# Kernel optimization log

Hardware: AMD Instinct MI355X
Metric: run time of the kernel (lower is better)

Reference implementation:

```python
import jax, jax.numpy as jnp
import numpy as np

H = 2048
EPS = 1e-5

def _layernorm(x, g, b):
    mu = jnp.mean(x, axis=-1, keepdims=True)
    var = jnp.mean(jnp.square(x - mu), axis=-1, keepdims=True)
    return (x - mu) * jax.lax.rsqrt(var + EPS) * g + b

def setup_inputs() -> dict:
    key = jax.random.key(0)
    ks = jax.random.split(key, 12)
    s = 1.0 / np.sqrt(H)
    inp = {
        "x": jax.random.normal(ks[0], (2, 2048, H), dtype=jnp.float32),
        "ln1_g": jnp.ones((H,), jnp.float32),
        "ln1_b": jnp.zeros((H,), jnp.float32),
        "ln2_g": jnp.ones((H,), jnp.float32),
        "ln2_b": jnp.zeros((H,), jnp.float32),
        "qkv_w": jax.random.uniform(ks[1], (H, 3 * H), jnp.float32, -s, s),
        "qkv_b": jax.random.uniform(ks[2], (3 * H,), jnp.float32, -s, s),
        "out_w": jax.random.uniform(ks[3], (H, H), jnp.float32, -s, s),
        "out_b": jax.random.uniform(ks[4], (H,), jnp.float32, -s, s),
        "mlp_w1": jax.random.uniform(ks[5], (H, 4 * H), jnp.float32, -s, s),
        "mlp_b1": jax.random.uniform(ks[6], (4 * H,), jnp.float32, -s, s),
        "mlp_w2": jax.random.uniform(ks[7], (4 * H, H), jnp.float32, -1.0 / np.sqrt(4 * H), 1.0 / np.sqrt(4 * H)),
        "mlp_b2": jax.random.uniform(ks[8], (H,), jnp.float32, -1.0 / np.sqrt(4 * H), 1.0 / np.sqrt(4 * H)),
    }
    return inp

def reference(x, ln1_g, ln1_b, ln2_g, ln2_b, qkv_w, qkv_b, out_w, out_b, mlp_w1, mlp_b1, mlp_w2, mlp_b2):
    residual = x
    h = _layernorm(x, ln1_g, ln1_b)
    qkv = h @ qkv_w + qkv_b                      # [B,S,3H]
    q, k, v = jnp.split(qkv, 3, axis=-1)         # each [B,S,H] (single-head attention)
    scores = jnp.einsum('bsh,bth->bst', q, k) / jnp.sqrt(jnp.float32(H))
    attn = jax.nn.softmax(scores, axis=-1)
    attn_out = jnp.einsum('bst,bth->bsh', attn, v)
    attn_out = attn_out @ out_w + out_b
    x = residual + attn_out                      # dropout is identity in eval
    residual = x
    h = _layernorm(x, ln2_g, ln2_b)
    h = jax.nn.gelu(h @ mlp_w1 + mlp_b1, approximate=False)
    h = h @ mlp_w2 + mlp_b2
    return residual + h
```

## Files before the change

kernel.cpp:

```cpp
#include <hip/hip_runtime.h>
#include <hip/hip_bf16.h>
#include <math.h>

typedef __bf16 bf16_t;
typedef __bf16 bf16x8 __attribute__((ext_vector_type(8)));
typedef __bf16 bf16x4 __attribute__((ext_vector_type(4)));
typedef float  f32x4  __attribute__((ext_vector_type(4)));

enum { EPI_BF16_BIAS = 0, EPI_F32_SCALE = 1, EPI_BF16 = 2, EPI_F32_BIAS_RES = 3, EPI_BF16_BIAS_GELU = 4 };

__device__ __forceinline__ float gelu_exact(float v) {
  return 0.5f * v * (1.0f + erff(v * 0.7071067811865476f));
}

__device__ __forceinline__ void gld_lds16(const bf16_t* g, bf16_t* l) {
  __builtin_amdgcn_global_load_lds(
      (const __attribute__((address_space(1))) uint32_t*)(uintptr_t)g,
      (__attribute__((address_space(3))) uint32_t*)(uintptr_t)l, 16, 0, 0);
}

#define SB()    __builtin_amdgcn_s_barrier()
#define SCHED() __builtin_amdgcn_sched_barrier(0)
#define VMW0()  asm volatile("s_waitcnt vmcnt(0)" ::: "memory")

template<int EPI, int ZDIV>
__global__ __launch_bounds__(512, 2) void tb_gemm8(
    const bf16_t* __restrict__ A, int lda, long long strideA, long long kofA,
    const bf16_t* __restrict__ B, int ldb, long long strideB, long long kofB,
    const float* __restrict__ bias,
    const float* __restrict__ resid,
    void* __restrict__ Cp, int ldc, long long strideC,
    int K, float scale)
{
  __shared__ __align__(16) bf16_t sm[65536];

  const int tid = threadIdx.x;
  const int lane = tid & 63;
  const int wid = tid >> 6;
  const int wm = wid >> 2;
  const int wn = wid & 3;
  const int lr = lane & 15;
  const int lg = lane >> 4;
  const int z = blockIdx.z;
  const int batch = z / ZDIV;
  const int ks = z % ZDIV;
  const int m0 = blockIdx.y * 256;
  const int n0 = blockIdx.x * 256;

  const bf16_t* Ag = A + (size_t)batch * strideA + (size_t)ks * kofA + (size_t)m0 * lda;
  const bf16_t* Bg = B + (size_t)batch * strideB + (size_t)ks * kofB + (size_t)n0 * ldb;

  const int l3 = lane >> 3;
  const int sl8 = ((lane & 7) ^ l3) << 3;

  f32x4 acc[8][4];
#pragma unroll
  for (int i = 0; i < 8; ++i)
#pragma unroll
    for (int j = 0; j < 4; ++j) acc[i][j] = (f32x4){0.f, 0.f, 0.f, 0.f};

  auto stage = [&](int par, int kt) {
    bf16_t* da = sm + (par << 15);
    bf16_t* db = da + 16384;
#pragma unroll
    for (int h = 0; h < 2; ++h)
#pragma unroll
      for (int q = 0; q < 2; ++q) {
        int c = (wid << 1) + q;
        int row = (h << 7) + (c << 3) + l3;
        gld_lds16(Ag + (size_t)row * lda + kt + sl8, da + (h << 13) + (c << 9) + lane * 8);
        gld_lds16(Bg + (size_t)row * ldb + kt + sl8, db + (h << 13) + (c << 9) + lane * 8);
      }
  };

#define RD(base, rowbase, kslot) \
  (*(const bf16x8*)((base) + ((rowbase) + lr) * 64 + (((((kslot) << 2) | lg)) ^ (lr & 7)) * 8))

  const int NT = K >> 6;
  stage(0, 0);
  VMW0();
  SB();

  for (int t = 0; t < NT; ++t) {
    SCHED();
    const bf16_t* cura = sm + ((t & 1) << 15);
    const bf16_t* curb = cura + 16384;
    if (t + 1 < NT) stage((t + 1) & 1, (t + 1) << 6);

    bf16x8 bF[4][2], aF[4][2];
#pragma unroll
    for (int jj = 0; jj < 4; ++jj) {
      bF[jj][0] = RD(curb, jj * 64 + wn * 16, 0);
      bF[jj][1] = RD(curb, jj * 64 + wn * 16, 1);
    }
#pragma unroll
    for (int ii = 0; ii < 4; ++ii) {
      aF[ii][0] = RD(cura, ii * 32 + wm * 16, 0);
      aF[ii][1] = RD(cura, ii * 32 + wm * 16, 1);
    }
    __builtin_amdgcn_s_setprio(1);
#pragma unroll
    for (int ii = 0; ii < 4; ++ii)
#pragma unroll
      for (int jj = 0; jj < 4; ++jj)
#pragma unroll
        for (int kk = 0; kk < 2; ++kk)
          acc[ii][jj] = __builtin_amdgcn_mfma_f32_16x16x32_bf16(aF[ii][kk], bF[jj][kk], acc[ii][jj], 0, 0, 0);
    __builtin_amdgcn_s_setprio(0);
#pragma unroll
    for (int ii = 0; ii < 4; ++ii) {
      aF[ii][0] = RD(cura, 128 + ii * 32 + wm * 16, 0);
      aF[ii][1] = RD(cura, 128 + ii * 32 + wm * 16, 1);
    }
    __builtin_amdgcn_s_setprio(1);
#pragma unroll
    for (int ii = 0; ii < 4; ++ii)
#pragma unroll
      for (int jj = 0; jj < 4; ++jj)
#pragma unroll
        for (int kk = 0; kk < 2; ++kk)
          acc[4 + ii][jj] = __builtin_amdgcn_mfma_f32_16x16x32_bf16(aF[ii][kk], bF[jj][kk], acc[4 + ii][jj], 0, 0, 0);
    __builtin_amdgcn_s_setprio(0);

    SCHED();
    if (t + 1 < NT) {
      VMW0();
      SB();
    }
  }
#undef RD

#pragma unroll
  for (int i = 0; i < 8; ++i) {
    const int mr = ((i >> 2) << 7) + ((i & 3) << 5) + (wm << 4);
#pragma unroll
    for (int j = 0; j < 4; ++j) {
      const int nc = j * 64 + (wn << 4);
#pragma unroll
      for (int r = 0; r < 4; ++r) {
        int row = m0 + mr + lg * 4 + r;
        int col = n0 + nc + lr;
        float v = acc[i][j][r] * scale;
        if constexpr (EPI == EPI_BF16_BIAS || EPI == EPI_F32_BIAS_RES || EPI == EPI_BF16_BIAS_GELU)
          v += bias[col];
        if constexpr (EPI == EPI_BF16_BIAS_GELU)
          v = gelu_exact(v);
        if constexpr (EPI == EPI_F32_BIAS_RES)
          v += resid[(size_t)row * ldc + col];
        if constexpr (EPI == EPI_BF16_BIAS || EPI == EPI_BF16 || EPI == EPI_BF16_BIAS_GELU) {
          ((bf16_t*)Cp)[(size_t)z * strideC + (size_t)row * ldc + col] = (bf16_t)v;
        } else {
          ((float*)Cp)[(size_t)z * strideC + (size_t)row * ldc + col] = v;
        }
      }
    }
  }
}

__global__ __launch_bounds__(256) void tb_combine(
    const float* __restrict__ x2, const float* __restrict__ p0,
    const float* __restrict__ p1, const float* __restrict__ bias,
    float* __restrict__ out)
{
  size_t o = ((size_t)blockIdx.x * 256 + threadIdx.x) * 4;
  float4 a = *(const float4*)(x2 + o);
  float4 b = *(const float4*)(p0 + o);
  float4 c = *(const float4*)(p1 + o);
  float4 bb = *(const float4*)(bias + (o & 2047));
  float4 r;
  r.x = a.x + b.x + c.x + bb.x;
  r.y = a.y + b.y + c.y + bb.y;
  r.z = a.z + b.z + c.z + bb.z;
  r.w = a.w + b.w + c.w + bb.w;
  *(float4*)(out + o) = r;
}

__global__ __launch_bounds__(256) void tb_combine_pv(
    const float* __restrict__ p, bf16_t* __restrict__ ao)
{
  size_t o = ((size_t)blockIdx.x * 256 + threadIdx.x) * 4;
  size_t b = o >> 22;
  size_t w = o & 4194303;
  const float* p0 = p + (b << 1) * 4194304 + w;
  const float* p1 = p0 + 4194304;
  float4 a = *(const float4*)p0;
  float4 c = *(const float4*)p1;
  bf16x4 r;
  r[0] = (bf16_t)(a.x + c.x);
  r[1] = (bf16_t)(a.y + c.y);
  r[2] = (bf16_t)(a.z + c.z);
  r[3] = (bf16_t)(a.w + c.w);
  *(bf16x4*)(ao + o) = r;
}

__global__ __launch_bounds__(256) void tb_transpose_cast(
    const float* __restrict__ in, bf16_t* __restrict__ outT, int R, int C)
{
  __shared__ float tile[32][33];
  int c0 = blockIdx.x * 32;
  int r0 = blockIdx.y * 32;
  int t = threadIdx.x;
  int r = t >> 3;
  int c4 = (t & 7) * 4;
  float4 d = *(const float4*)(in + (size_t)(r0 + r) * C + c0 + c4);
  tile[r][c4 + 0] = d.x; tile[r][c4 + 1] = d.y; tile[r][c4 + 2] = d.z; tile[r][c4 + 3] = d.w;
  __syncthreads();
  int c = t >> 3;
  int r4 = (t & 7) * 4;
  bf16x4 o;
  o[0] = (bf16_t)tile[r4 + 0][c];
  o[1] = (bf16_t)tile[r4 + 1][c];
  o[2] = (bf16_t)tile[r4 + 2][c];
  o[3] = (bf16_t)tile[r4 + 3][c];
  *(bf16x4*)(outT + (size_t)(c0 + c) * R + r0 + r4) = o;
}

__global__ __launch_bounds__(256) void tb_transpose_bf16(
    const bf16_t* __restrict__ in, int ldin, long long sIn,
    bf16_t* __restrict__ out, int ldout, long long sOut)
{
  __shared__ bf16_t tile[32][40];
  int z = blockIdx.z;
  const bf16_t* src = in + (size_t)z * sIn;
  bf16_t* dst = out + (size_t)z * sOut;
  int c0 = blockIdx.x * 32;
  int r0 = blockIdx.y * 32;
  int t = threadIdx.x;
  int r = t >> 3;
  int c4 = (t & 7) * 4;
  bf16x4 d = *(const bf16x4*)(src + (size_t)(r0 + r) * ldin + c0 + c4);
  *(bf16x4*)&tile[r][c4] = d;
  __syncthreads();
  int c = t >> 3;
  int r4 = (t & 7) * 4;
  bf16x4 o;
  o[0] = tile[r4 + 0][c];
  o[1] = tile[r4 + 1][c];
  o[2] = tile[r4 + 2][c];
  o[3] = tile[r4 + 3][c];
  *(bf16x4*)(dst + (size_t)(c0 + c) * ldout + r0 + r4) = o;
}

__global__ __launch_bounds__(256) void tb_layernorm(
    const float* __restrict__ x, const float* __restrict__ g, const float* __restrict__ b,
    bf16_t* __restrict__ h)
{
  __shared__ float sa[4], sb[4];
  int row = blockIdx.x;
  int t = threadIdx.x;
  const float* xr = x + (size_t)row * 2048;
  float4 v0 = *(const float4*)(xr + t * 8);
  float4 v1 = *(const float4*)(xr + t * 8 + 4);
  float a[8] = {v0.x, v0.y, v0.z, v0.w, v1.x, v1.y, v1.z, v1.w};
  float s = 0.f, q = 0.f;
#pragma unroll
  for (int j = 0; j < 8; ++j) { s += a[j]; q += a[j] * a[j]; }
#pragma unroll
  for (int o = 32; o; o >>= 1) { s += __shfl_down(s, o); q += __shfl_down(q, o); }
  int w = t >> 6, l = t & 63;
  if (l == 0) { sa[w] = s; sb[w] = q; }
  __syncthreads();
  if (t == 0) {
    sa[0] = sa[0] + sa[1] + sa[2] + sa[3];
    sb[0] = sb[0] + sb[1] + sb[2] + sb[3];
  }
  __syncthreads();
  float mu = sa[0] * (1.0f / 2048.0f);
  float var = sb[0] * (1.0f / 2048.0f) - mu * mu;
  float rs = rsqrtf(var + 1e-5f);
  float4 g0 = *(const float4*)(g + t * 8);
  float4 g1 = *(const float4*)(g + t * 8 + 4);
  float4 b0 = *(const float4*)(b + t * 8);
  float4 b1 = *(const float4*)(b + t * 8 + 4);
  float gv[8] = {g0.x, g0.y, g0.z, g0.w, g1.x, g1.y, g1.z, g1.w};
  float bv[8] = {b0.x, b0.y, b0.z, b0.w, b1.x, b1.y, b1.z, b1.w};
  bf16x8 o8;
#pragma unroll
  for (int j = 0; j < 8; ++j) o8[j] = (bf16_t)((a[j] - mu) * rs * gv[j] + bv[j]);
  *(bf16x8*)(h + (size_t)row * 2048 + t * 8) = o8;
}

__global__ __launch_bounds__(256) void tb_softmax_add(
    const float* __restrict__ p, bf16_t* __restrict__ P)
{
  __shared__ float sa[4];
  int row = blockIdx.x;
  int t = threadIdx.x;
  size_t base = ((size_t)(row >> 11) * 2) * 4194304 + (size_t)(row & 2047) * 2048;
  const float* p0 = p + base;
  const float* p1 = p0 + 4194304;
  float4 a0 = *(const float4*)(p0 + t * 8);
  float4 a1 = *(const float4*)(p0 + t * 8 + 4);
  float4 c0 = *(const float4*)(p1 + t * 8);
  float4 c1 = *(const float4*)(p1 + t * 8 + 4);
  float v[8] = {a0.x + c0.x, a0.y + c0.y, a0.z + c0.z, a0.w + c0.w,
                a1.x + c1.x, a1.y + c1.y, a1.z + c1.z, a1.w + c1.w};
  float m = v[0];
#pragma unroll
  for (int j = 1; j < 8; ++j) m = fmaxf(m, v[j]);
#pragma unroll
  for (int o = 32; o; o >>= 1) m = fmaxf(m, __shfl_down(m, o));
  int w = t >> 6, l = t & 63;
  if (l == 0) sa[w] = m;
  __syncthreads();
  if (t == 0) sa[0] = fmaxf(fmaxf(sa[0], sa[1]), fmaxf(sa[2], sa[3]));
  __syncthreads();
  m = sa[0];
  __syncthreads();
  float s = 0.f;
#pragma unroll
  for (int j = 0; j < 8; ++j) { v[j] = expf(v[j] - m); s += v[j]; }
#pragma unroll
  for (int o = 32; o; o >>= 1) s += __shfl_down(s, o);
  if (l == 0) sa[w] = s;
  __syncthreads();
  if (t == 0) sa[0] = sa[0] + sa[1] + sa[2] + sa[3];
  __syncthreads();
  float inv = 1.0f / sa[0];
  bf16x8 o8;
#pragma unroll
  for (int j = 0; j < 8; ++j) o8[j] = (bf16_t)(v[j] * inv);
  *(bf16x8*)(P + (size_t)row * 2048 + t * 8) = o8;
}

extern "C" void kernel_launch(void* const* d_in, const int* in_sizes, int n_in,
                              void* d_out, int out_size, void* d_ws, size_t ws_size,
                              hipStream_t stream) {
  const float* x     = (const float*)d_in[0];
  const float* ln1_g = (const float*)d_in[1];
  const float* ln1_b = (const float*)d_in[2];
  const float* ln2_g = (const float*)d_in[3];
  const float* ln2_b = (const float*)d_in[4];
  const float* qkv_w = (const float*)d_in[5];
  const float* qkv_b = (const float*)d_in[6];
  const float* out_w = (const float*)d_in[7];
  const float* out_b = (const float*)d_in[8];
  const float* w1    = (const float*)d_in[9];
  const float* b1    = (const float*)d_in[10];
  const float* w2    = (const float*)d_in[11];
  const float* b2    = (const float*)d_in[12];
  float* out = (float*)d_out;
  char* ws = (char*)d_ws;

  float*  sp     = (float*)(ws + 0);
  bf16_t* qkv_wT = (bf16_t*)(ws + 0);
  bf16_t* out_wT = (bf16_t*)(ws + 67108864);
  bf16_t* w1T    = (bf16_t*)(ws + 75497472);
  bf16_t* w2T    = (bf16_t*)(ws + 109051904);
  bf16_t* h_bf   = (bf16_t*)(ws + 142606336);
  bf16_t* qkv_bf = (bf16_t*)(ws + 159383552);
  bf16_t* mid_bf = (bf16_t*)(ws + 159383552);
  bf16_t* attn_bf= (bf16_t*)(ws + 209715200);
  bf16_t* Vt     = (bf16_t*)(ws + 226492416);
  bf16_t* ao_bf  = (bf16_t*)(ws + 243269632);
  float*  x2     = (float*)(ws + 226492416);

  const float inv_sqrt_h = 0.022097086912079608f;

  tb_transpose_cast<<<dim3(6144 / 32, 2048 / 32), 256, 0, stream>>>(qkv_w, qkv_wT, 2048, 6144);
  tb_transpose_cast<<<dim3(2048 / 32, 2048 / 32), 256, 0, stream>>>(out_w, out_wT, 2048, 2048);
  tb_transpose_cast<<<dim3(8192 / 32, 2048 / 32), 256, 0, stream>>>(w1, w1T, 2048, 8192);
  tb_transpose_cast<<<dim3(2048 / 32, 8192 / 32), 256, 0, stream>>>(w2, w2T, 8192, 2048);

  tb_layernorm<<<4096, 256, 0, stream>>>(x, ln1_g, ln1_b, h_bf);

  tb_gemm8<EPI_BF16_BIAS, 1><<<dim3(24, 16, 1), 512, 0, stream>>>(
      h_bf, 2048, 0, 0, qkv_wT, 2048, 0, 0, qkv_b, nullptr, qkv_bf, 6144, 0, 2048, 1.0f);

  tb_transpose_bf16<<<dim3(64, 64, 2), 256, 0, stream>>>(
      qkv_bf + 4096, 6144, 2048LL * 6144, Vt, 2048, 2048LL * 2048);

  tb_gemm8<EPI_F32_SCALE, 2><<<dim3(8, 8, 4), 512, 0, stream>>>(
      qkv_bf, 6144, 2048LL * 6144, 1024, qkv_bf + 2048, 6144, 2048LL * 6144, 1024,
      nullptr, nullptr, sp, 2048, 4194304LL, 1024, inv_sqrt_h);

  tb_softmax_add<<<4096, 256, 0, stream>>>(sp, attn_bf);

  tb_gemm8<EPI_F32_SCALE, 2><<<dim3(8, 8, 4), 512, 0, stream>>>(
      attn_bf, 2048, 2048LL * 2048, 1024, Vt, 2048, 2048LL * 2048, 1024,
      nullptr, nullptr, sp, 2048, 4194304LL, 1024, 1.0f);

  tb_combine_pv<<<8192, 256, 0, stream>>>(sp, ao_bf);

  tb_gemm8<EPI_F32_SCALE, 2><<<dim3(8, 16, 2), 512, 0, stream>>>(
      ao_bf, 2048, 0, 1024, out_wT, 2048, 0, 1024,
      nullptr, nullptr, sp, 2048, 8388608LL, 1024, 1.0f);

  tb_combine<<<8192, 256, 0, stream>>>(x, sp, sp + 8388608, out_b, x2);

  tb_layernorm<<<4096, 256, 0, stream>>>(x2, ln2_g, ln2_b, h_bf);

  tb_gemm8<EPI_BF16_BIAS_GELU, 1><<<dim3(32, 16, 1), 512, 0, stream>>>(
      h_bf, 2048, 0, 0, w1T, 2048, 0, 0, b1, nullptr, mid_bf, 8192, 0, 2048, 1.0f);

  tb_gemm8<EPI_F32_SCALE, 2><<<dim3(8, 16, 2), 512, 0, stream>>>(
      mid_bf, 8192, 0, 4096, w2T, 8192, 0, 4096,
      nullptr, nullptr, sp, 2048, 8388608LL, 4096, 1.0f);

  tb_combine<<<8192, 256, 0, stream>>>(x2, sp, sp + 8388608, b2, out);
}
```

Baseline: 686.3 us.

## Store split-K partials in bf16 and fuse residual combine with second layernorm

Split-K GEMM partial outputs (scores, PV, out-proj, MLP down) are now written as bf16 instead of fp32. The reduction kernels (softmax, PV combine, final combine) read bf16 and sum in fp32, halving partial-sum traffic. The out-proj combine is also fused with the second layernorm, removing one kernel and one pass over x2. The cost is lower precision for the partial sums, including attention scores and the residual-stream contributions.

```diff
diff --git a/kernel.cpp b/kernel.cpp
--- a/kernel.cpp
+++ b/kernel.cpp
@@ -157,40 +157,100 @@
   }
 }
 
-__global__ __launch_bounds__(256) void tb_combine(
-    const float* __restrict__ x2, const float* __restrict__ p0,
-    const float* __restrict__ p1, const float* __restrict__ bias,
-    float* __restrict__ out)
-{
-  size_t o = ((size_t)blockIdx.x * 256 + threadIdx.x) * 4;
-  float4 a = *(const float4*)(x2 + o);
-  float4 b = *(const float4*)(p0 + o);
-  float4 c = *(const float4*)(p1 + o);
-  float4 bb = *(const float4*)(bias + (o & 2047));
-  float4 r;
-  r.x = a.x + b.x + c.x + bb.x;
-  r.y = a.y + b.y + c.y + bb.y;
-  r.z = a.z + b.z + c.z + bb.z;
-  r.w = a.w + b.w + c.w + bb.w;
-  *(float4*)(out + o) = r;
+__global__ __launch_bounds__(256) void tb_combine_f(
+    const float* __restrict__ x2, const bf16_t* __restrict__ p,
+    const float* __restrict__ bias, float* __restrict__ out)
+{
+  size_t o = ((size_t)blockIdx.x * 256 + threadIdx.x) * 8;
+  float4 a0 = *(const float4*)(x2 + o);
+  float4 a1 = *(const float4*)(x2 + o + 4);
+  bf16x8 pa = *(const bf16x8*)(p + o);
+  bf16x8 pb = *(const bf16x8*)(p + 8388608 + o);
+  size_t c = o & 2047;
+  float4 b0 = *(const float4*)(bias + c);
+  float4 b1 = *(const float4*)(bias + c + 4);
+  float4 r0, r1;
+  r0.x = a0.x + (float)pa[0] + (float)pb[0] + b0.x;
+  r0.y = a0.y + (float)pa[1] + (float)pb[1] + b0.y;
+  r0.z = a0.z + (float)pa[2] + (float)pb[2] + b0.z;
+  r0.w = a0.w + (float)pa[3] + (float)pb[3] + b0.w;
+  r1.x = a1.x + (float)pa[4] + (float)pb[4] + b1.x;
+  r1.y = a1.y + (float)pa[5] + (float)pb[5] + b1.y;
+  r1.z = a1.z + (float)pa[6] + (float)pb[6] + b1.z;
+  r1.w = a1.w + (float)pa[7] + (float)pb[7] + b1.w;
+  *(float4*)(out + o) = r0;
+  *(float4*)(out + o + 4) = r1;
 }
 
 __global__ __launch_bounds__(256) void tb_combine_pv(
-    const float* __restrict__ p, bf16_t* __restrict__ ao)
-{
-  size_t o = ((size_t)blockIdx.x * 256 + threadIdx.x) * 4;
+    const bf16_t* __restrict__ p, bf16_t* __restrict__ ao)
+{
+  size_t o = ((size_t)blockIdx.x * 256 + threadIdx.x) * 8;
   size_t b = o >> 22;
   size_t w = o & 4194303;
-  const float* p0 = p + (b << 1) * 4194304 + w;
-  const float* p1 = p0 + 4194304;
-  float4 a = *(const float4*)p0;
-  float4 c = *(const float4*)p1;
-  bf16x4 r;
-  r[0] = (bf16_t)(a.x + c.x);
-  r[1] = (bf16_t)(a.y + c.y);
-  r[2] = (bf16_t)(a.z + c.z);
-  r[3] = (bf16_t)(a.w + c.w);
-  *(bf16x4*)(ao + o) = r;
+  const bf16_t* p0 = p + (b << 1) * 4194304 + w;
+  const bf16_t* p1 = p0 + 4194304;
+  bf16x8 a = *(const bf16x8*)p0;
+  bf16x8 c = *(const bf16x8*)p1;
+  bf16x8 r;
+#pragma unroll
+  for (int j = 0; j < 8; ++j) r[j] = (bf16_t)((float)a[j] + (float)c[j]);
+  *(bf16x8*)(ao + o) = r;
+}
+
+__global__ __launch_bounds__(256) void tb_combine_ln(
+    const float* __restrict__ x, const bf16_t* __restrict__ p,
+    const float* __restrict__ ob,
+    const float* __restrict__ g, const float* __restrict__ b,
+    float* __restrict__ x2, bf16_t* __restrict__ h)
+{
+  __shared__ float sa[4], sb[4];
+  int row = blockIdx.x;
+  int t = threadIdx.x;
+  const float* xr = x + (size_t)row * 2048;
+  const bf16_t* p0 = p + (size_t)row * 2048;
+  const bf16_t* p1 = p0 + 8388608;
+  float4 v0 = *(const float4*)(xr + t * 8);
+  float4 v1 = *(const float4*)(xr + t * 8 + 4);
+  bf16x8 pa = *(const bf16x8*)(p0 + t * 8);
+  bf16x8 pb = *(const bf16x8*)(p1 + t * 8);
+  float4 o0 = *(const float4*)(ob + t * 8);
+  float4 o1 = *(const float4*)(ob + t * 8 + 4);
+  float a[8] = {v0.x, v0.y, v0.z, v0.w, v1.x, v1.y, v1.z, v1.w};
+  float ov[8] = {o0.x, o0.y, o0.z, o0.w, o1.x, o1.y, o1.z, o1.w};
+  float s = 0.f, q = 0.f;
+#pragma unroll
+  for (int j = 0; j < 8; ++j) {
+    a[j] += (float)pa[j] + (float)pb[j] + ov[j];
+    s += a[j]; q += a[j] * a[j];
+  }
+  float4 w0 = {a[0], a[1], a[2], a[3]};
+  float4 w1 = {a[4], a[5], a[6], a[7]};
+  *(float4*)(x2 + (size_t)row * 2048 + t * 8) = w0;
+  *(float4*)(x2 + (size_t)row * 2048 + t * 8 + 4) = w1;
+#pragma unroll
+  for (int o = 32; o; o >>= 1) { s += __shfl_down(s, o); q += __shfl_down(q, o); }
+  int w = t >> 6, l = t & 63;
+  if (l == 0) { sa[w] = s; sb[w] = q; }
+  __syncthreads();
+  if (t == 0) {
+    sa[0] = sa[0] + sa[1] + sa[2] + sa[3];
+    sb[0] = sb[0] + sb[1] + sb[2] + sb[3];
+  }
+  __syncthreads();
+  float mu = sa[0] * (1.0f / 2048.0f);
+  float var = sb[0] * (1.0f / 2048.0f) - mu * mu;
+  float rs = rsqrtf(var + 1e-5f);
+  float4 g0 = *(const float4*)(g + t * 8);
+  float4 g1 = *(const float4*)(g + t * 8 + 4);
+  float4 b0 = *(const float4*)(b + t * 8);
+  float4 b1 = *(const float4*)(b + t * 8 + 4);
+  float gv[8] = {g0.x, g0.y, g0.z, g0.w, g1.x, g1.y, g1.z, g1.w};
+  float bv[8] = {b0.x, b0.y, b0.z, b0.w, b1.x, b1.y, b1.z, b1.w};
+  bf16x8 o8;
+#pragma unroll
+  for (int j = 0; j < 8; ++j) o8[j] = (bf16_t)((a[j] - mu) * rs * gv[j] + bv[j]);
+  *(bf16x8*)(h + (size_t)row * 2048 + t * 8) = o8;
 }
 
 __global__ __launch_bounds__(256) void tb_transpose_cast(
@@ -281,20 +341,19 @@
 }
 
 __global__ __launch_bounds__(256) void tb_softmax_add(
-    const float* __restrict__ p, bf16_t* __restrict__ P)
+    const bf16_t* __restrict__ p, bf16_t* __restrict__ P)
 {
   __shared__ float sa[4];
   int row = blockIdx.x;
   int t = threadIdx.x;
   size_t base = ((size_t)(row >> 11) * 2) * 4194304 + (size_t)(row & 2047) * 2048;
-  const float* p0 = p + base;
-  const float* p1 = p0 + 4194304;
-  float4 a0 = *(const float4*)(p0 + t * 8);
-  float4 a1 = *(const float4*)(p0 + t * 8 + 4);
-  float4 c0 = *(const float4*)(p1 + t * 8);
-  float4 c1 = *(const float4*)(p1 + t * 8 + 4);
-  float v[8] = {a0.x + c0.x, a0.y + c0.y, a0.z + c0.z, a0.w + c0.w,
-                a1.x + c1.x, a1.y + c1.y, a1.z + c1.z, a1.w + c1.w};
+  const bf16_t* p0 = p + base;
+  const bf16_t* p1 = p0 + 4194304;
+  bf16x8 a = *(const bf16x8*)(p0 + t * 8);
+  bf16x8 c = *(const bf16x8*)(p1 + t * 8);
+  float v[8];
+#pragma unroll
+  for (int j = 0; j < 8; ++j) v[j] = (float)a[j] + (float)c[j];
   float m = v[0];
 #pragma unroll
   for (int j = 1; j < 8; ++j) m = fmaxf(m, v[j]);
@@ -342,7 +401,7 @@
   float* out = (float*)d_out;
   char* ws = (char*)d_ws;
 
-  float*  sp     = (float*)(ws + 0);
+  bf16_t* spb    = (bf16_t*)(ws + 0);
   bf16_t* qkv_wT = (bf16_t*)(ws + 0);
   bf16_t* out_wT = (bf16_t*)(ws + 67108864);
   bf16_t* w1T    = (bf16_t*)(ws + 75497472);
@@ -370,32 +429,30 @@
   tb_transpose_bf16<<<dim3(64, 64, 2), 256, 0, stream>>>(
       qkv_bf + 4096, 6144, 2048LL * 6144, Vt, 2048, 2048LL * 2048);
 
-  tb_gemm8<EPI_F32_SCALE, 2><<<dim3(8, 8, 4), 512, 0, stream>>>(
+  tb_gemm8<EPI_BF16, 2><<<dim3(8, 8, 4), 512, 0, stream>>>(
       qkv_bf, 6144, 2048LL * 6144, 1024, qkv_bf + 2048, 6144, 2048LL * 6144, 1024,
-      nullptr, nullptr, sp, 2048, 4194304LL, 1024, inv_sqrt_h);
-
-  tb_softmax_add<<<4096, 256, 0, stream>>>(sp, attn_bf);
-
-  tb_gemm8<EPI_F32_SCALE, 2><<<dim3(8, 8, 4), 512, 0, stream>>>(
+      nullptr, nullptr, spb, 2048, 4194304LL, 1024, inv_sqrt_h);
+
+  tb_softmax_add<<<4096, 256, 0, stream>>>(spb, attn_bf);
+
+  tb_gemm8<EPI_BF16, 2><<<dim3(8, 8, 4), 512, 0, stream>>>(
       attn_bf, 2048, 2048LL * 2048, 1024, Vt, 2048, 2048LL * 2048, 1024,
-      nullptr, nullptr, sp, 2048, 4194304LL, 1024, 1.0f);
-
-  tb_combine_pv<<<8192, 256, 0, stream>>>(sp, ao_bf);
-
-  tb_gemm8<EPI_F32_SCALE, 2><<<dim3(8, 16, 2), 512, 0, stream>>>(
+      nullptr, nullptr, spb, 2048, 4194304LL, 1024, 1.0f);
+
+  tb_combine_pv<<<4096, 256, 0, stream>>>(spb, ao_bf);
+
+  tb_gemm8<EPI_BF16, 2><<<dim3(8, 16, 2), 512, 0, stream>>>(
       ao_bf, 2048, 0, 1024, out_wT, 2048, 0, 1024,
-      nullptr, nullptr, sp, 2048, 8388608LL, 1024, 1.0f);
-
-  tb_combine<<<8192, 256, 0, stream>>>(x, sp, sp + 8388608, out_b, x2);
-
-  tb_layernorm<<<4096, 256, 0, stream>>>(x2, ln2_g, ln2_b, h_bf);
+      nullptr, nullptr, spb, 2048, 8388608LL, 1024, 1.0f);
+
+  tb_combine_ln<<<4096, 256, 0, stream>>>(x, spb, out_b, ln2_g, ln2_b, x2, h_bf);
 
   tb_gemm8<EPI_BF16_BIAS_GELU, 1><<<dim3(32, 16, 1), 512, 0, stream>>>(
       h_bf, 2048, 0, 0, w1T, 2048, 0, 0, b1, nullptr, mid_bf, 8192, 0, 2048, 1.0f);
 
-  tb_gemm8<EPI_F32_SCALE, 2><<<dim3(8, 16, 2), 512, 0, stream>>>(
+  tb_gemm8<EPI_BF16, 2><<<dim3(8, 16, 2), 512, 0, stream>>>(
       mid_bf, 8192, 0, 4096, w2T, 8192, 0, 4096,
-      nullptr, nullptr, sp, 2048, 8388608LL, 4096, 1.0f);
-
-  tb_combine<<<8192, 256, 0, stream>>>(x2, sp, sp + 8388608, b2, out);
-}
+      nullptr, nullptr, spb, 2048, 8388608LL, 4096, 1.0f);
+
+  tb_combine_f<<<4096, 256, 0, stream>>>(x2, spb, b2, out);
+}
```

After: 656.9 us. 4.3% less time.
